# Kernel optimization log

Measured on AMD Instinct MI355X. Metric: run time of the kernel, lower is better.

Reference implementation:

```python
import jax, jax.numpy as jnp
import numpy as np

BN_EPS = 1e-5

def setup_inputs() -> dict:
    key = jax.random.key(0)
    k1, k2, k3, k4 = jax.random.split(key, 4)
    B, Cin, Cout, H, Wd, K = 8, 128, 128, 256, 256, 64
    x = jax.random.normal(k1, (B, Cin, H, Wd), dtype=jnp.float32)
    index = jax.random.randint(k2, (B, 1, H, Wd), 0, K, dtype=jnp.int32)
    weight = jax.random.normal(k3, (Cin, Cout), dtype=jnp.float32) * 0.1
    W = jax.random.normal(k4, (Cout, Cout), dtype=jnp.float32) * 0.1
    adj_mask = jnp.ones((K, K), dtype=jnp.float32)
    gamma = jnp.ones((Cout,), dtype=jnp.float32)
    beta = jnp.zeros((Cout,), dtype=jnp.float32)
    return {"x": x, "index": index, "weight": weight, "W": W,
            "adj_mask": adj_mask, "gamma": gamma, "beta": beta}


def reference(x, index, weight, W, adj_mask, gamma, beta):
    # x: [B, Cin, H, W]; index: [B, 1, H, W] block ids in [0, K)
    B = x.shape[0]
    K = adj_mask.shape[0]
    # linear feature transform
    xw = jnp.einsum('bchw,cd->bdhw', x, weight)          # [B, Cout, H, W]
    idx = index[:, 0]                                     # [B, H, W] (nearest upsample to same size = identity)
    oh = jax.nn.one_hot(idx, K, dtype=xw.dtype)           # [B, H, W, K]
    counts = jnp.sum(oh, axis=(1, 2))                     # [B, K]
    sums = jnp.einsum('bhwk,bdhw->bkd', oh, xw)           # segment sums [B, K, Cout]
    denom = counts + (counts == 0).astype(xw.dtype)
    means = sums / denom[..., None]                       # segment means [B, K, Cout]
    # pairwise differences D[b,p,q,:] = means[b,q] - means[b,p]
    D = means[:, None, :, :] - means[:, :, None, :]       # [B, K, K, Cout]
    M = W @ W.T                                           # PSD bilinear form
    quad = jnp.einsum('bpqc,cd,bpqd->bpq', D, M, D)       # [B, K, K]
    adj = jnp.exp(-quad) + jnp.eye(K, dtype=xw.dtype)
    adj = adj * adj_mask
    # aggregate neighbor means (zero diagonal)
    adj_nd = adj * (1.0 - jnp.eye(K, dtype=xw.dtype))
    adj_means = jnp.einsum('bpq,bqd->bpd', adj_nd, means)  # [B, K, Cout]
    # scatter aggregated block features back to pixels and add residual
    features = xw + jnp.einsum('bhwk,bkd->bdhw', oh, adj_means)
    # BatchNorm2d (training-mode batch statistics, biased variance)
    mu = features.mean(axis=(0, 2, 3), keepdims=True)
    var = features.var(axis=(0, 2, 3), keepdims=True)
    out = (features - mu) / jnp.sqrt(var + BN_EPS)
    out = out * gamma.reshape(1, -1, 1, 1) + beta.reshape(1, -1, 1, 1)
    return out
```

## Files before the change

### kernel.cpp

```cpp
#include <hip/hip_runtime.h>
#include <math.h>

typedef __attribute__((ext_vector_type(8))) short bf16x8;
typedef __attribute__((ext_vector_type(4))) float f32x4;

namespace {
constexpr int BB = 8, CH = 128, KC = 64, HWD = 65536;
constexpr int TILE = 64;
constexpr int TPB  = 256;
constexpr int TILES_PER_BLOCK = 16;
constexpr int PX_PER_BLOCK = TILE * TILES_PER_BLOCK;
constexpr int BLOCKS_PER_B = HWD / PX_PER_BLOCK;
constexpr int XS_STRIDE = 136;

constexpr int OFF_SUMS  = 0;
constexpr int OFF_CNT   = OFF_SUMS + BB*KC*CH;
constexpr int OFF_CHSQ  = OFF_CNT + BB*KC;
constexpr int OFF_AM    = OFF_CHSQ + CH;
constexpr int OFF_SCALE = OFF_AM + BB*KC*CH;
constexpr int OFF_BIAS  = OFF_SCALE + CH;
constexpr int OFF_AMSB  = OFF_BIAS + CH;
}

__device__ __forceinline__ short f2bf(float f) {
  unsigned u = __builtin_bit_cast(unsigned, f);
  u += 0x7fffu + ((u >> 16) & 1u);
  return (short)(u >> 16);
}

__device__ __forceinline__ void load_w_frags(const float* __restrict__ w,
                                             int mbase, int lane15, int quad,
                                             bf16x8 af[4][4]) {
#pragma unroll
  for (int mt = 0; mt < 4; ++mt) {
    const int d = mbase + mt * 16 + lane15;
#pragma unroll
    for (int kc = 0; kc < 4; ++kc) {
      const int c0 = kc * 32 + quad * 8;
      bf16x8 f;
#pragma unroll
      for (int j = 0; j < 8; ++j) f[j] = f2bf(w[(size_t)(c0 + j) * CH + d]);
      af[mt][kc] = f;
    }
  }
}

__device__ __forceinline__ void stage_x(const float* __restrict__ xb, int pix0,
                                        short* __restrict__ xs, int t) {
  const int p0 = (t & 15) * 4, c0 = (t >> 4) * 8;
  float4 v[8];
#pragma unroll
  for (int j = 0; j < 8; ++j)
    v[j] = *(const float4*)&xb[(size_t)(c0 + j) * HWD + pix0 + p0];
#pragma unroll
  for (int pp = 0; pp < 4; ++pp) {
    bf16x8 f;
#pragma unroll
    for (int j = 0; j < 8; ++j) f[j] = f2bf(((const float*)&v[j])[pp]);
    *(bf16x8*)&xs[(p0 + pp) * XS_STRIDE + c0] = f;
  }
}

__global__ __launch_bounds__(TPB) void k1_mfma(
    const float* __restrict__ x, const int* __restrict__ index,
    const float* __restrict__ weight, float* __restrict__ ws)
{
  __shared__ short xs[TILE * XS_STRIDE];
  __shared__ float csum[KC][CH + 1];
  __shared__ float ccnt[KC];
  __shared__ float chsq_s[CH];

  const int t = threadIdx.x;
  const int lane = t & 63, lane15 = lane & 15, quad = lane >> 4, w = t >> 6;
  const int mbase = (w & 1) * 64;
  const int nbase = (w >> 1) * 32;
  const int b = blockIdx.x / BLOCKS_PER_B;
  const int px_base = (blockIdx.x % BLOCKS_PER_B) * PX_PER_BLOCK;

  for (int i = t; i < KC * (CH + 1); i += TPB) (&csum[0][0])[i] = 0.f;
  if (t < KC) ccnt[t] = 0.f;
  if (t < CH) chsq_s[t] = 0.f;

  bf16x8 af[4][4];
  load_w_frags(weight, mbase, lane15, quad, af);

  float sq[4][4] = {};
  const float* xb = x + (size_t)b * CH * HWD;
  const int*   ib = index + (size_t)b * HWD;
  __syncthreads();

  for (int tile = 0; tile < TILES_PER_BLOCK; ++tile) {
    const int pix0 = px_base + tile * TILE;
    stage_x(xb, pix0, xs, t);
    __syncthreads();

    int cls[2];
#pragma unroll
    for (int nt = 0; nt < 2; ++nt) cls[nt] = ib[pix0 + nbase + nt * 16 + lane15];

    f32x4 acc[4][2] = {};
#pragma unroll
    for (int kc = 0; kc < 4; ++kc) {
      bf16x8 bfr[2];
#pragma unroll
      for (int nt = 0; nt < 2; ++nt)
        bfr[nt] = *(const bf16x8*)&xs[(nbase + nt * 16 + lane15) * XS_STRIDE + kc * 32 + quad * 8];
#pragma unroll
      for (int mt = 0; mt < 4; ++mt)
#pragma unroll
        for (int nt = 0; nt < 2; ++nt)
          acc[mt][nt] = __builtin_amdgcn_mfma_f32_16x16x32_bf16(af[mt][kc], bfr[nt], acc[mt][nt], 0, 0, 0);
    }

#pragma unroll
    for (int nt = 0; nt < 2; ++nt) {
      float* cr = &csum[cls[nt]][0];
#pragma unroll
      for (int mt = 0; mt < 4; ++mt)
#pragma unroll
        for (int r = 0; r < 4; ++r) {
          const float v = acc[mt][nt][r];
          atomicAdd(&cr[mbase + mt * 16 + quad * 4 + r], v);
          sq[mt][r] += v * v;
        }
    }
    if ((w & 1) == 0 && lane < 16) {
      atomicAdd(&ccnt[cls[0]], 1.f);
      atomicAdd(&ccnt[cls[1]], 1.f);
    }
    __syncthreads();
  }

  float* sums_g = ws + OFF_SUMS + (size_t)b * KC * CH;
  for (int i = t; i < KC * CH; i += TPB)
    atomicAdd(&sums_g[i], csum[i >> 7][i & 127]);
#pragma unroll
  for (int mt = 0; mt < 4; ++mt)
#pragma unroll
    for (int r = 0; r < 4; ++r)
      atomicAdd(&chsq_s[mbase + mt * 16 + quad * 4 + r], sq[mt][r]);
  __syncthreads();
  if (t < KC) atomicAdd(&ws[OFF_CNT + b * KC + t], ccnt[t]);
  if (t < CH) atomicAdd(&ws[OFF_CHSQ + t], chsq_s[t]);
}

__global__ __launch_bounds__(TPB) void k2_adj(
    const float* __restrict__ Wm, const float* __restrict__ adj_mask,
    float* __restrict__ ws)
{
  __shared__ float ms[KC][CH + 1];
  __shared__ float Ys[KC][CH + 1];
  __shared__ float wm[KC][KC];
  __shared__ float yy[KC];
  const int b = blockIdx.x, t = threadIdx.x;
  const float* sums = ws + OFF_SUMS + (size_t)b * KC * CH;
  const float* cnt  = ws + OFF_CNT + b * KC;

  for (int i = t; i < KC * CH; i += TPB) {
    const int k = i >> 7, d = i & 127;
    const float c = cnt[k];
    ms[k][d] = sums[i] / (c == 0.f ? 1.f : c);
  }
  __syncthreads();
  for (int i = t; i < KC * CH; i += TPB) {
    const int k = i >> 7, e = i & 127;
    float a = 0.f;
    for (int c = 0; c < CH; ++c) a += ms[k][c] * Wm[c * CH + e];
    Ys[k][e] = a;
  }
  __syncthreads();
  if (t < KC) {
    float a = 0.f;
    for (int e = 0; e < CH; ++e) { const float v = Ys[t][e]; a += v * v; }
    yy[t] = a;
  }
  __syncthreads();
  for (int i = t; i < KC * KC; i += TPB) {
    const int p = i >> 6, q = i & 63;
    float g = 0.f;
    for (int e = 0; e < CH; ++e) g += Ys[p][e] * Ys[q][e];
    const float quad = yy[p] + yy[q] - 2.f * g;
    wm[p][q] = (p == q) ? 0.f : expf(-quad) * adj_mask[i];
  }
  __syncthreads();
  float* am = ws + OFF_AM + (size_t)b * KC * CH;
  for (int i = t; i < KC * CH; i += TPB) {
    const int p = i >> 7, d = i & 127;
    float a = 0.f;
    for (int q = 0; q < KC; ++q) a += wm[p][q] * ms[q][d];
    am[i] = a;
  }
}

__global__ __launch_bounds__(CH) void k3_bn(
    const float* __restrict__ gamma, const float* __restrict__ beta,
    float* __restrict__ ws)
{
  const int d = threadIdx.x;
  float chs = 0.f, cm = 0.f, cam2 = 0.f, cross = 0.f;
  for (int bk = 0; bk < BB * KC; ++bk) {
    const float c = ws[OFF_CNT + bk];
    const float a = ws[OFF_AM + (size_t)bk * CH + d];
    const float s = ws[OFF_SUMS + (size_t)bk * CH + d];
    chs += s; cm += c * a; cam2 += c * a * a; cross += a * s;
  }
  const float N   = (float)BB * (float)HWD;
  const float mu  = (chs + cm) / N;
  const float e2  = (ws[OFF_CHSQ + d] + 2.f * cross + cam2) / N;
  const float var = e2 - mu * mu;
  const float sc  = gamma[d] / sqrtf(var + 1e-5f);
  const float bi  = beta[d] - mu * sc;
  if (blockIdx.x == 0) { ws[OFF_SCALE + d] = sc; ws[OFF_BIAS + d] = bi; }
  for (int r = 0; r < 8; ++r) {
    const int bk = blockIdx.x * 8 + r;
    ws[OFF_AMSB + (size_t)bk * CH + d] = ws[OFF_AM + (size_t)bk * CH + d] * sc + bi;
  }
}

__global__ __launch_bounds__(TPB) void k4_mfma(
    const float* __restrict__ x, const int* __restrict__ index,
    const float* __restrict__ weight, const float* __restrict__ ws,
    float* __restrict__ out)
{
  __shared__ short xs[TILE * XS_STRIDE];
  __shared__ float amsb[KC][CH + 4];

  const int t = threadIdx.x;
  const int lane = t & 63, lane15 = lane & 15, quad = lane >> 4, w = t >> 6;
  const int mbase = (w & 1) * 64;
  const int nbase = (w >> 1) * 32;
  const int b = blockIdx.x / BLOCKS_PER_B;
  const int px_base = (blockIdx.x % BLOCKS_PER_B) * PX_PER_BLOCK;

  const float* ag = ws + OFF_AMSB + (size_t)b * KC * CH;
  for (int i = t; i < KC * CH / 4; i += TPB) {
    const int k = (i * 4) >> 7, dd = (i * 4) & 127;
    *(float4*)&amsb[k][dd] = *(const float4*)&ag[k * CH + dd];
  }

  bf16x8 af[4][4];
  load_w_frags(weight, mbase, lane15, quad, af);

  float scr[4][4];
#pragma unroll
  for (int mt = 0; mt < 4; ++mt)
#pragma unroll
    for (int r = 0; r < 4; ++r)
      scr[mt][r] = ws[OFF_SCALE + mbase + mt * 16 + quad * 4 + r];

  const float* xb = x + (size_t)b * CH * HWD;
  const int*   ib = index + (size_t)b * HWD;
  float*       ob = out + (size_t)b * CH * HWD;
  __syncthreads();

  for (int tile = 0; tile < TILES_PER_BLOCK; ++tile) {
    const int pix0 = px_base + tile * TILE;
    stage_x(xb, pix0, xs, t);
    __syncthreads();

    int cls[2];
#pragma unroll
    for (int nt = 0; nt < 2; ++nt) cls[nt] = ib[pix0 + nbase + nt * 16 + lane15];

    f32x4 acc[4][2] = {};
#pragma unroll
    for (int kc = 0; kc < 4; ++kc) {
      bf16x8 bfr[2];
#pragma unroll
      for (int nt = 0; nt < 2; ++nt)
        bfr[nt] = *(const bf16x8*)&xs[(nbase + nt * 16 + lane15) * XS_STRIDE + kc * 32 + quad * 8];
#pragma unroll
      for (int mt = 0; mt < 4; ++mt)
#pragma unroll
        for (int nt = 0; nt < 2; ++nt)
          acc[mt][nt] = __builtin_amdgcn_mfma_f32_16x16x32_bf16(af[mt][kc], bfr[nt], acc[mt][nt], 0, 0, 0);
    }

#pragma unroll
    for (int nt = 0; nt < 2; ++nt) {
      const float* ar = &amsb[cls[nt]][0];
      const int px = pix0 + nbase + nt * 16 + lane15;
#pragma unroll
      for (int mt = 0; mt < 4; ++mt)
#pragma unroll
        for (int r = 0; r < 4; ++r) {
          const int d = mbase + mt * 16 + quad * 4 + r;
          ob[(size_t)d * HWD + px] = acc[mt][nt][r] * scr[mt][r] + ar[d];
        }
    }
    __syncthreads();
  }
}

extern "C" void kernel_launch(void* const* d_in, const int* in_sizes, int n_in,
                              void* d_out, int out_size, void* d_ws, size_t ws_size,
                              hipStream_t stream) {
  const float* x        = (const float*)d_in[0];
  const int*   index    = (const int*)d_in[1];
  const float* weight   = (const float*)d_in[2];
  const float* Wm       = (const float*)d_in[3];
  const float* adj_mask = (const float*)d_in[4];
  const float* gamma    = (const float*)d_in[5];
  const float* beta     = (const float*)d_in[6];
  float* ws  = (float*)d_ws;
  float* out = (float*)d_out;

  hipMemsetAsync(ws, 0, (size_t)OFF_AM * sizeof(float), stream);

  k1_mfma<<<BB * BLOCKS_PER_B, TPB, 0, stream>>>(x, index, weight, ws);
  k2_adj <<<BB, TPB, 0, stream>>>(Wm, adj_mask, ws);
  k3_bn  <<<KC, CH, 0, stream>>>(gamma, beta, ws);
  k4_mfma<<<BB * BLOCKS_PER_B, TPB, 0, stream>>>(x, index, weight, ws, out);
}
```

Measured before the change: 970.7 us.

## Pre-pack x to swizzled bf16 tiles and async double-buffer LDS loads

Adds a packing kernel that converts x once to bf16 in a swizzled per-tile layout in workspace. Both GEMM kernels then stage tiles with global_load_lds DMA into double-buffered LDS, so they no longer do per-tile fp32 loads and conversions. k4 batches four tiles of accumulators before writing output, and k1 rotates its global atomic order across blocks to cut contention. This adds an extra pass writing a packed copy of x, and relies on barriers covering the async LDS loads.

Result: slower. 1.071 ms (+10.3%).

```diff
diff --git a/kernel.cpp b/kernel.cpp
--- a/kernel.cpp
+++ b/kernel.cpp
@@ -11,7 +11,7 @@
 constexpr int TILES_PER_BLOCK = 16;
 constexpr int PX_PER_BLOCK = TILE * TILES_PER_BLOCK;
 constexpr int BLOCKS_PER_B = HWD / PX_PER_BLOCK;
-constexpr int XS_STRIDE = 136;
+constexpr int TILE_BYTES = 16384;
 
 constexpr int OFF_SUMS  = 0;
 constexpr int OFF_CNT   = OFF_SUMS + BB*KC*CH;
@@ -20,6 +20,7 @@
 constexpr int OFF_SCALE = OFF_AM + BB*KC*CH;
 constexpr int OFF_BIAS  = OFF_SCALE + CH;
 constexpr int OFF_AMSB  = OFF_BIAS + CH;
+constexpr int OFF_XP    = OFF_AMSB + BB*KC*CH;
 }
 
 __device__ __forceinline__ short f2bf(float f) {
@@ -28,6 +29,29 @@
   return (short)(u >> 16);
 }
 
+__device__ __forceinline__ void gload_lds16(const void* g, void* l) {
+  __builtin_amdgcn_global_load_lds(
+      (const __attribute__((address_space(1))) unsigned*)g,
+      (__attribute__((address_space(3))) unsigned*)l, 16, 0, 0);
+}
+
+__device__ __forceinline__ void stage_tile(const char* __restrict__ gsrc,
+                                           short* __restrict__ dst,
+                                           int w, int lane) {
+#pragma unroll
+  for (int i = 0; i < 4; ++i) {
+    const int c = (w * 4 + i) * 1024;
+    gload_lds16(gsrc + c + lane * 16, (char*)dst + c);
+  }
+}
+
+__device__ __forceinline__ bf16x8 bfrag(const char* __restrict__ xt,
+                                        int pxl, int kc, int quad) {
+  const int cc   = kc * 2 + (quad >> 1);
+  const int slot = (quad & 1) ^ ((pxl >> 2) & 1);
+  return *(const bf16x8*)(xt + cc * 2048 + pxl * 32 + (slot << 4));
+}
+
 __device__ __forceinline__ void load_w_frags(const float* __restrict__ w,
                                              int mbase, int lane15, int quad,
                                              bf16x8 af[4][4]) {
@@ -45,27 +69,49 @@
   }
 }
 
-__device__ __forceinline__ void stage_x(const float* __restrict__ xb, int pix0,
-                                        short* __restrict__ xs, int t) {
-  const int p0 = (t & 15) * 4, c0 = (t >> 4) * 8;
-  float4 v[8];
-#pragma unroll
-  for (int j = 0; j < 8; ++j)
-    v[j] = *(const float4*)&xb[(size_t)(c0 + j) * HWD + pix0 + p0];
-#pragma unroll
-  for (int pp = 0; pp < 4; ++pp) {
-    bf16x8 f;
-#pragma unroll
-    for (int j = 0; j < 8; ++j) f[j] = f2bf(((const float*)&v[j])[pp]);
-    *(bf16x8*)&xs[(p0 + pp) * XS_STRIDE + c0] = f;
+__global__ __launch_bounds__(TPB) void k0_pack(const float* __restrict__ x,
+                                               float* __restrict__ ws)
+{
+  char* xp = (char*)(ws + OFF_XP);
+  const int blk = blockIdx.x;
+  const int b   = blk >> 8;
+  const int pg  = (blk >> 2) & 63;
+  const int cc0 = (blk & 3) * 2;
+  const int t = threadIdx.x;
+  const int o = t >> 7;
+  const int g = t & 127;
+  const int px0 = pg * PX_PER_BLOCK;
+  const float* xb = x + (size_t)b * CH * HWD;
+
+#pragma unroll
+  for (int cci = 0; cci < 2; ++cci) {
+    const int cc = cc0 + cci;
+    float4 v[8][2];
+#pragma unroll
+    for (int r = 0; r < 8; ++r) {
+      const float* row = &xb[(size_t)(cc * 16 + o * 8 + r) * HWD + px0 + g * 8];
+      v[r][0] = *(const float4*)row;
+      v[r][1] = *(const float4*)(row + 4);
+    }
+#pragma unroll
+    for (int k = 0; k < 8; ++k) {
+      bf16x8 wv;
+#pragma unroll
+      for (int r = 0; r < 8; ++r)
+        wv[r] = f2bf(((const float*)&v[r][k >> 2])[k & 3]);
+      const int px = px0 + g * 8 + k;
+      const size_t ti = (size_t)b * 1024 + (px >> 6);
+      const int slot = o ^ ((px >> 2) & 1);
+      *(bf16x8*)(xp + ti * TILE_BYTES + cc * 2048 + (px & 63) * 32 + (slot << 4)) = wv;
+    }
   }
 }
 
 __global__ __launch_bounds__(TPB) void k1_mfma(
-    const float* __restrict__ x, const int* __restrict__ index,
+    const int* __restrict__ index,
     const float* __restrict__ weight, float* __restrict__ ws)
 {
-  __shared__ short xs[TILE * XS_STRIDE];
+  __shared__ short xs[2][TILE_BYTES / 2];
   __shared__ float csum[KC][CH + 1];
   __shared__ float ccnt[KC];
   __shared__ float chsq_s[CH];
@@ -76,6 +122,8 @@
   const int nbase = (w >> 1) * 32;
   const int b = blockIdx.x / BLOCKS_PER_B;
   const int px_base = (blockIdx.x % BLOCKS_PER_B) * PX_PER_BLOCK;
+  const size_t ti0 = (size_t)b * 1024 + (px_base >> 6);
+  const char* xp = (const char*)(ws + OFF_XP);
 
   for (int i = t; i < KC * (CH + 1); i += TPB) (&csum[0][0])[i] = 0.f;
   if (t < KC) ccnt[t] = 0.f;
@@ -85,26 +133,29 @@
   load_w_frags(weight, mbase, lane15, quad, af);
 
   float sq[4][4] = {};
-  const float* xb = x + (size_t)b * CH * HWD;
-  const int*   ib = index + (size_t)b * HWD;
+  const int* ib = index + (size_t)b * HWD;
+
+  stage_tile(xp + ti0 * TILE_BYTES, &xs[0][0], w, lane);
   __syncthreads();
 
   for (int tile = 0; tile < TILES_PER_BLOCK; ++tile) {
+    const int cur = tile & 1;
+    if (tile + 1 < TILES_PER_BLOCK)
+      stage_tile(xp + (ti0 + tile + 1) * TILE_BYTES, &xs[cur ^ 1][0], w, lane);
+
     const int pix0 = px_base + tile * TILE;
-    stage_x(xb, pix0, xs, t);
-    __syncthreads();
-
     int cls[2];
 #pragma unroll
     for (int nt = 0; nt < 2; ++nt) cls[nt] = ib[pix0 + nbase + nt * 16 + lane15];
 
+    const char* xt = (const char*)&xs[cur][0];
     f32x4 acc[4][2] = {};
 #pragma unroll
     for (int kc = 0; kc < 4; ++kc) {
       bf16x8 bfr[2];
 #pragma unroll
       for (int nt = 0; nt < 2; ++nt)
-        bfr[nt] = *(const bf16x8*)&xs[(nbase + nt * 16 + lane15) * XS_STRIDE + kc * 32 + quad * 8];
+        bfr[nt] = bfrag(xt, nbase + nt * 16 + lane15, kc, quad);
 #pragma unroll
       for (int mt = 0; mt < 4; ++mt)
 #pragma unroll
@@ -132,8 +183,11 @@
   }
 
   float* sums_g = ws + OFF_SUMS + (size_t)b * KC * CH;
-  for (int i = t; i < KC * CH; i += TPB)
-    atomicAdd(&sums_g[i], csum[i >> 7][i & 127]);
+  const int rot = (blockIdx.x & 63) * 131;
+  for (int i = t; i < KC * CH; i += TPB) {
+    const int ii = (i + rot) & (KC * CH - 1);
+    atomicAdd(&sums_g[ii], csum[ii >> 7][ii & 127]);
+  }
 #pragma unroll
   for (int mt = 0; mt < 4; ++mt)
 #pragma unroll
@@ -217,12 +271,12 @@
   }
 }
 
-__global__ __launch_bounds__(TPB) void k4_mfma(
-    const float* __restrict__ x, const int* __restrict__ index,
+__global__ __launch_bounds__(TPB, 2) void k4_mfma(
+    const int* __restrict__ index,
     const float* __restrict__ weight, const float* __restrict__ ws,
     float* __restrict__ out)
 {
-  __shared__ short xs[TILE * XS_STRIDE];
+  __shared__ short xs[2][TILE_BYTES / 2];
   __shared__ float amsb[KC][CH + 4];
 
   const int t = threadIdx.x;
@@ -231,6 +285,8 @@
   const int nbase = (w >> 1) * 32;
   const int b = blockIdx.x / BLOCKS_PER_B;
   const int px_base = (blockIdx.x % BLOCKS_PER_B) * PX_PER_BLOCK;
+  const size_t ti0 = (size_t)b * 1024 + (px_base >> 6);
+  const char* xp = (const char*)(ws + OFF_XP);
 
   const float* ag = ws + OFF_AMSB + (size_t)b * KC * CH;
   for (int i = t; i < KC * CH / 4; i += TPB) {
@@ -248,47 +304,60 @@
     for (int r = 0; r < 4; ++r)
       scr[mt][r] = ws[OFF_SCALE + mbase + mt * 16 + quad * 4 + r];
 
-  const float* xb = x + (size_t)b * CH * HWD;
-  const int*   ib = index + (size_t)b * HWD;
-  float*       ob = out + (size_t)b * CH * HWD;
-  __syncthreads();
-
-  for (int tile = 0; tile < TILES_PER_BLOCK; ++tile) {
-    const int pix0 = px_base + tile * TILE;
-    stage_x(xb, pix0, xs, t);
-    __syncthreads();
-
-    int cls[2];
-#pragma unroll
-    for (int nt = 0; nt < 2; ++nt) cls[nt] = ib[pix0 + nbase + nt * 16 + lane15];
-
-    f32x4 acc[4][2] = {};
-#pragma unroll
-    for (int kc = 0; kc < 4; ++kc) {
-      bf16x8 bfr[2];
+  const int* ib = index + (size_t)b * HWD;
+  float*     ob = out + (size_t)b * CH * HWD;
+
+  stage_tile(xp + ti0 * TILE_BYTES, &xs[0][0], w, lane);
+  __syncthreads();
+
+#pragma unroll
+  for (int g4 = 0; g4 < 4; ++g4) {
+    f32x4 acc[4][4][2] = {};
+    int clsv[4][2];
+#pragma unroll
+    for (int g = 0; g < 4; ++g) {
+      const int tile = g4 * 4 + g;
+      const int cur = tile & 1;
+      if (tile + 1 < TILES_PER_BLOCK)
+        stage_tile(xp + (ti0 + tile + 1) * TILE_BYTES, &xs[cur ^ 1][0], w, lane);
+
+      const int pix0 = px_base + tile * TILE;
 #pragma unroll
       for (int nt = 0; nt < 2; ++nt)
-        bfr[nt] = *(const bf16x8*)&xs[(nbase + nt * 16 + lane15) * XS_STRIDE + kc * 32 + quad * 8];
-#pragma unroll
-      for (int mt = 0; mt < 4; ++mt)
+        clsv[g][nt] = ib[pix0 + nbase + nt * 16 + lane15];
+
+      const char* xt = (const char*)&xs[cur][0];
+#pragma unroll
+      for (int kc = 0; kc < 4; ++kc) {
+        bf16x8 bfr[2];
 #pragma unroll
         for (int nt = 0; nt < 2; ++nt)
-          acc[mt][nt] = __builtin_amdgcn_mfma_f32_16x16x32_bf16(af[mt][kc], bfr[nt], acc[mt][nt], 0, 0, 0);
-    }
-
-#pragma unroll
-    for (int nt = 0; nt < 2; ++nt) {
-      const float* ar = &amsb[cls[nt]][0];
-      const int px = pix0 + nbase + nt * 16 + lane15;
-#pragma unroll
-      for (int mt = 0; mt < 4; ++mt)
-#pragma unroll
-        for (int r = 0; r < 4; ++r) {
-          const int d = mbase + mt * 16 + quad * 4 + r;
-          ob[(size_t)d * HWD + px] = acc[mt][nt][r] * scr[mt][r] + ar[d];
-        }
-    }
-    __syncthreads();
+          bfr[nt] = bfrag(xt, nbase + nt * 16 + lane15, kc, quad);
+#pragma unroll
+        for (int mt = 0; mt < 4; ++mt)
+#pragma unroll
+          for (int nt = 0; nt < 2; ++nt)
+            acc[g][mt][nt] = __builtin_amdgcn_mfma_f32_16x16x32_bf16(af[mt][kc], bfr[nt], acc[g][mt][nt], 0, 0, 0);
+      }
+      __syncthreads();
+    }
+
+    const int pxg = px_base + g4 * 256;
+#pragma unroll
+    for (int mt = 0; mt < 4; ++mt)
+#pragma unroll
+      for (int r = 0; r < 4; ++r) {
+        const int d = mbase + mt * 16 + quad * 4 + r;
+        const float sc = scr[mt][r];
+        float* obd = ob + (size_t)d * HWD;
+#pragma unroll
+        for (int g = 0; g < 4; ++g)
+#pragma unroll
+          for (int nt = 0; nt < 2; ++nt) {
+            const int px = pxg + g * 64 + nbase + nt * 16 + lane15;
+            obd[px] = acc[g][mt][nt][r] * sc + amsb[clsv[g][nt]][d];
+          }
+      }
   }
 }
 
@@ -304,11 +373,13 @@
   const float* beta     = (const float*)d_in[6];
   float* ws  = (float*)d_ws;
   float* out = (float*)d_out;
+  (void)ws_size;
 
   hipMemsetAsync(ws, 0, (size_t)OFF_AM * sizeof(float), stream);
 
-  k1_mfma<<<BB * BLOCKS_PER_B, TPB, 0, stream>>>(x, index, weight, ws);
+  k0_pack<<<BB * 256, TPB, 0, stream>>>(x, ws);
+  k1_mfma<<<BB * BLOCKS_PER_B, TPB, 0, stream>>>(index, weight, ws);
   k2_adj <<<BB, TPB, 0, stream>>>(Wm, adj_mask, ws);
   k3_bn  <<<KC, CH, 0, stream>>>(gamma, beta, ws);
-  k4_mfma<<<BB * BLOCKS_PER_B, TPB, 0, stream>>>(x, index, weight, ws, out);
-}
+  k4_mfma<<<BB * BLOCKS_PER_B, TPB, 0, stream>>>(index, weight, ws, out);
+}
```
